# Kernel optimization log

Hardware: AMD Instinct MI355X
Metric: run time of the kernel (lower is better)

## Reference

```python
import jax, jax.numpy as jnp
import numpy as np

TOTAL_WORDS = 10000
EMBED_LEN = 100
SEQ_LEN = 80
BATCH = 2048
UNITS = 1024


def setup_inputs() -> dict:
    key = jax.random.key(0)
    ks = jax.random.split(key, 8)
    inputs = jax.random.randint(ks[0], (BATCH, SEQ_LEN), 0, TOTAL_WORDS)
    s = 0.02
    emb = jax.random.normal(ks[1], (TOTAL_WORDS, EMBED_LEN), jnp.float32) * s
    W0 = jax.random.normal(ks[2], (EMBED_LEN, 4 * UNITS), jnp.float32) * s
    U0 = jax.random.normal(ks[3], (UNITS, 4 * UNITS), jnp.float32) * s
    b0 = jnp.zeros((4 * UNITS,), jnp.float32)
    W1 = jax.random.normal(ks[4], (UNITS, 4 * UNITS), jnp.float32) * s
    U1 = jax.random.normal(ks[5], (UNITS, 4 * UNITS), jnp.float32) * s
    b1 = jnp.zeros((4 * UNITS,), jnp.float32)
    fcW = jax.random.normal(ks[6], (UNITS, 1), jnp.float32) * s
    fcb = jnp.zeros((1,), jnp.float32)
    return {"inputs": inputs, "emb": emb, "W0": W0, "U0": U0, "b0": b0,
            "W1": W1, "U1": U1, "b1": b1, "fcW": fcW, "fcb": fcb}


def _lstm_step(x, h, c, W, U, b):
    # Keras LSTMCell gate order: i, f, g(candidate), o
    z = x @ W + h @ U + b  # [B, 4*units]
    i, f, g, o = jnp.split(z, 4, axis=-1)
    i = jax.nn.sigmoid(i)
    f = jax.nn.sigmoid(f)
    g = jnp.tanh(g)
    o = jax.nn.sigmoid(o)
    c_new = f * c + i * g
    h_new = o * jnp.tanh(c_new)
    return h_new, c_new


def reference(inputs, emb, W0, U0, b0, W1, U1, b1, fcW, fcb):
    x = emb[inputs]                      # [B, T, E]
    xs = jnp.transpose(x, (1, 0, 2))     # [T, B, E] for scan over time
    B = inputs.shape[0]
    U = U0.shape[0]
    init = (jnp.zeros((B, U), x.dtype), jnp.zeros((B, U), x.dtype),
            jnp.zeros((B, U), x.dtype), jnp.zeros((B, U), x.dtype))

    def step(carry, xt):
        h0, c0, h1, c1 = carry
        h0, c0 = _lstm_step(xt, h0, c0, W0, U0, b0)
        h1, c1 = _lstm_step(h0, h1, c1, W1, U1, b1)
        return (h0, c0, h1, c1), None

    (h0, c0, h1, c1), _ = jax.lax.scan(step, init, xs)
    logits = h1 @ fcW + fcb              # [B, 1]
    return jax.nn.sigmoid(logits)
```

## Files before the change

kernel.cpp:

```cpp
#include <hip/hip_runtime.h>

#define DEVI __device__ __forceinline__

typedef __attribute__((ext_vector_type(4))) float f4;
typedef long long i64t;

DEVI unsigned char f2fp8(float x) {
  int p = __builtin_amdgcn_cvt_pk_fp8_f32(x, x, 0, false);
  return (unsigned char)(p & 0xff);
}
DEVI float fp82f(unsigned char b) {
  return __builtin_amdgcn_cvt_f32_fp8((int)b, 0);
}
DEVI float sigmoidf_(float x) { return 1.f / (1.f + __expf(-x)); }
DEVI float tanhf_(float x) {
  float ax = fabsf(x);
  float e = __expf(-2.f * ax);
  float t = (1.f - e) / (1.f + e);
  return x < 0.f ? -t : t;
}

#define GLDS16(g, l) __builtin_amdgcn_global_load_lds( \
    (const __attribute__((address_space(1))) void*)(g), \
    (__attribute__((address_space(3))) void*)(l), 16, 0, 0)

#define SCALE_UP 64.0f
#define SCALE_DN (1.0f / 4096.0f)


__global__ void k_conv_emb(const float* __restrict__ emb, unsigned char* __restrict__ ep) {
  int i = blockIdx.x * 256 + threadIdx.x;
  if (i >= 10000 * 128) return;
  int r = i >> 7, c = i & 127;
  ep[i] = (c < 100) ? f2fp8(emb[r * 100 + c] * SCALE_UP) : (unsigned char)0;
}

DEVI int permn(int n) {
  int g = n >> 10, u = n & 1023;
  return (u >> 5) * 128 + ((u >> 4) & 1) * 64 + g * 16 + (u & 15);
}
DEVI int kswz(int klog, int row) {
  return (klog & ~63) | ((((klog >> 4) & 3) ^ ((row >> 2) & 3)) << 4) | (klog & 15);
}

__global__ void k_conv_w0(const float* __restrict__ W0, const float* __restrict__ U0,
                          unsigned char* __restrict__ WT) {
  int i = blockIdx.x * 256 + threadIdx.x;
  if (i >= 4096 * 1152) return;
  int n = i / 1152, k = i - n * 1152;
  float v;
  if (k < 100) v = W0[k * 4096 + n];
  else if (k < 128) v = 0.f;
  else v = U0[(k - 128) * 4096 + n];
  int np = permn(n);
  WT[(size_t)np * 1152 + kswz(k, np)] = f2fp8(v * SCALE_UP);
}

__global__ void k_conv_w1(const float* __restrict__ W1, const float* __restrict__ U1,
                          unsigned char* __restrict__ WT) {
  int i = blockIdx.x * 256 + threadIdx.x;
  if (i >= 4096 * 2048) return;
  int n = i >> 11, k = i & 2047;
  float v = (k < 1024) ? W1[k * 4096 + n] : U1[(k - 1024) * 4096 + n];
  int np = permn(n);
  WT[(size_t)np * 2048 + kswz(k, np)] = f2fp8(v * SCALE_UP);
}


template<int K1, int KTOT, bool GATHER>
DEVI void lstm_body(int tile, char* smem,
    const unsigned char* __restrict__ src1,
    const unsigned char* __restrict__ src2,
    const int* __restrict__ idx, int t,
    const unsigned char* __restrict__ WT,
    const float* __restrict__ bias,
    float* __restrict__ cbuf,
    unsigned char* __restrict__ hout)
{
  const int tid = threadIdx.x;
  const int bn = tile & 31;
  const int bm = tile >> 5;
  const int m0 = bm * 256;
  const int n0 = bn * 128;

  const int lr = tid >> 2;
  const int c16 = (tid & 3) * 16;
  const int csw = (((tid & 3) ^ ((tid >> 4) & 3))) * 16;

  const unsigned char* g1[2];
  if (GATHER) {
#pragma unroll
    for (int p = 0; p < 2; ++p) {
      int w = idx[(m0 + p * 128 + lr) * 80 + t];
      g1[p] = src1 + (size_t)w * K1 + csw;
    }
  }

  char* const LA0 = smem;
  char* const LB0 = smem + 16384;
  char* const LA1 = smem + 24576;
  char* const LB1 = smem + 40960;

  auto stage = [&](int kb) {
    char* la = (kb & 1) ? LA1 : LA0;
    char* lb = (kb & 1) ? LB1 : LB0;
    const int kc = kb * 64;
    if (GATHER && kc < K1) {
#pragma unroll
      for (int p = 0; p < 2; ++p)
        GLDS16(g1[p] + kc, la + p * 8192 + tid * 16);
    } else {
#pragma unroll
      for (int p = 0; p < 2; ++p) {
        size_t row = (size_t)(m0 + p * 128 + lr);
        const unsigned char* g = (kc < K1)
            ? (src1 + row * 1024 + kc + c16)
            : (src2 + row * 1024 + (kc - K1) + c16);
        GLDS16(g, la + p * 8192 + tid * 16);
      }
    }
    GLDS16(WT + (size_t)(n0 + lr) * KTOT + kc + c16, lb + tid * 16);
  };

  const int lane = tid & 63;
  const int wv = tid >> 6;
  const int wm = wv >> 1;
  const int wn = wv & 1;
  const int cl = lane & 15;
  const int qd = lane >> 4;
  const int qh = qd >> 1, qb = qd & 1;
  const int fcl = (cl >> 2) & 3;
  const int koff0 = ((qh ^ fcl) << 4) + qb * 8;
  const int koff1 = (((2 + qh) ^ fcl) << 4) + qb * 8;

  f4 acc[4][4];
  const f4 fz = {0.f, 0.f, 0.f, 0.f};
#pragma unroll
  for (int a = 0; a < 4; ++a)
#pragma unroll
    for (int b = 0; b < 4; ++b) acc[a][b] = fz;

  stage(0);

  constexpr int NKB = KTOT / 64;
#pragma unroll 1
  for (int kb = 0; kb < NKB; ++kb) {
    __syncthreads();
    if (kb + 1 < NKB) stage(kb + 1);
    char* la = (kb & 1) ? LA1 : LA0;
    char* lb = (kb & 1) ? LB1 : LB0;
#pragma unroll
    for (int kk = 0; kk < 2; ++kk) {
      const int ko = kk ? koff1 : koff0;
      i64t af[4], bfr[4];
#pragma unroll
      for (int mi = 0; mi < 4; ++mi)
        af[mi] = *(const i64t*)(la + (wm * 64 + mi * 16 + cl) * 64 + ko);
#pragma unroll
      for (int j = 0; j < 4; ++j)
        bfr[j] = *(const i64t*)(lb + (wn * 64 + j * 16 + cl) * 64 + ko);
#pragma unroll
      for (int mi = 0; mi < 4; ++mi)
#pragma unroll
        for (int j = 0; j < 4; ++j)
          acc[mi][j] = __builtin_amdgcn_mfma_f32_16x16x32_fp8_fp8(
              af[mi], bfr[j], acc[mi][j], 0, 0, 0);
    }
  }

  const int u = bn * 32 + wn * 16 + cl;
  const int hcol = (u & ~63) | (((((u >> 4) & 3) ^ qd)) << 4) | (u & 15);
  const float bi = bias[u];
  const float bff = bias[1024 + u];
  const float bg = bias[2048 + u];
  const float bo = bias[3072 + u];
#pragma unroll
  for (int mi = 0; mi < 4; ++mi) {
    int mbase = m0 + wm * 64 + mi * 16 + qd * 4;
#pragma unroll
    for (int r = 0; r < 4; ++r) {
      int m = mbase + r;
      float gi = sigmoidf_(acc[mi][0][r] * SCALE_DN + bi);
      float gf = sigmoidf_(acc[mi][1][r] * SCALE_DN + bff);
      float gg = tanhf_(acc[mi][2][r] * SCALE_DN + bg);
      float go = sigmoidf_(acc[mi][3][r] * SCALE_DN + bo);
      size_t coff = (size_t)m * 1024 + u;
      float cn = gf * cbuf[coff] + gi * gg;
      cbuf[coff] = cn;
      hout[(size_t)m * 1024 + hcol] = f2fp8(go * tanhf_(cn) * SCALE_UP);
    }
  }
}

__global__ __launch_bounds__(512, 4) void k_step(
    int mode,
    const unsigned char* embp, const unsigned char* h0in,
    const int* idx, int t,
    const unsigned char* WT0, const float* b0, float* c0, unsigned char* h0out,
    const unsigned char* h0prev, const unsigned char* h1in,
    const unsigned char* WT1, const float* b1, float* c1, unsigned char* h1out)
{
  extern __shared__ char smem[];
  const int blk = blockIdx.x;
  int tile;
  bool isL0;
  if (mode == 1) {
    int hi = (blk >> 8) & 1;
    isL0 = ((blk & 1) ^ hi) != 0;
    tile = hi * 128 + ((blk & 255) >> 1);
  } else {
    tile = blk;
    isL0 = (mode == 0);
  }
  if (isL0)
    lstm_body<128, 1152, true>(tile, smem, embp, h0in, idx, t,
                               WT0, b0, c0, h0out);
  else
    lstm_body<1024, 2048, false>(tile, smem, h0prev, h1in, nullptr, 0,
                                 WT1, b1, c1, h1out);
}


__global__ void k_fc(const unsigned char* __restrict__ h1,
                     const float* __restrict__ fcW, const float* __restrict__ fcb,
                     float* __restrict__ out) {
  int wv = threadIdx.x >> 6;
  int lane = threadIdx.x & 63;
  int row = blockIdx.x * 4 + wv;
  if (row >= 2048) return;
  const unsigned char* hr = h1 + (size_t)row * 1024;
  const int f = (row >> 2) & 3;
  float s = 0.f;
  for (int k = lane; k < 1024; k += 64) {
    int ks = (k & ~63) | ((((k >> 4) & 3) ^ f) << 4) | (k & 15);
    s += fp82f(hr[ks]) * fcW[k];
  }
#pragma unroll
  for (int off = 32; off > 0; off >>= 1) s += __shfl_down(s, off);
  if (lane == 0) out[row] = sigmoidf_(s * (1.0f / SCALE_UP) + fcb[0]);
}


extern "C" void kernel_launch(void* const* d_in, const int* in_sizes, int n_in,
                              void* d_out, int out_size, void* d_ws, size_t ws_size,
                              hipStream_t stream) {
  const int*   idx = (const int*)d_in[0];
  const float* emb = (const float*)d_in[1];
  const float* W0  = (const float*)d_in[2];
  const float* U0  = (const float*)d_in[3];
  const float* b0  = (const float*)d_in[4];
  const float* W1  = (const float*)d_in[5];
  const float* U1  = (const float*)d_in[6];
  const float* b1  = (const float*)d_in[7];
  const float* fcW = (const float*)d_in[8];
  const float* fcb = (const float*)d_in[9];
  float* out = (float*)d_out;

  char* ws = (char*)d_ws;
  unsigned char* embp = (unsigned char*)(ws);
  unsigned char* WT0  = (unsigned char*)(ws + 1280000);
  unsigned char* WT1  = (unsigned char*)(ws + 5998592);
  unsigned char* h0b[2] = {(unsigned char*)(ws + 14387200),
                           (unsigned char*)(ws + 16484352)};
  unsigned char* h1b[2] = {(unsigned char*)(ws + 18581504),
                           (unsigned char*)(ws + 20678656)};
  float* c0 = (float*)(ws + 22775808);
  float* c1 = (float*)(ws + 31164416);

  hipMemsetAsync(ws + 14387200, 0, 25165824, stream);

  k_conv_emb<<<5000, 256, 0, stream>>>(emb, embp);
  k_conv_w0<<<18432, 256, 0, stream>>>(W0, U0, WT0);
  k_conv_w1<<<32768, 256, 0, stream>>>(W1, U1, WT1);

  k_step<<<256, 512, 49152, stream>>>(0, embp, h0b[1], idx, 0,
                                      WT0, b0, c0, h0b[0],
                                      nullptr, nullptr, WT1, b1, c1, nullptr);
  for (int t = 1; t < 80; ++t) {
    k_step<<<512, 512, 49152, stream>>>(1, embp, h0b[(t + 1) & 1], idx, t,
                                        WT0, b0, c0, h0b[t & 1],
                                        h0b[(t - 1) & 1], h1b[t & 1],
                                        WT1, b1, c1, h1b[(t + 1) & 1]);
  }
  k_step<<<256, 512, 49152, stream>>>(2, nullptr, nullptr, nullptr, 0,
                                      WT0, b0, c0, nullptr,
                                      h0b[1], h1b[0], WT1, b1, c1, h1b[1]);

  k_fc<<<512, 256, 0, stream>>>(h1b[1], fcW, fcb, out);
}
```

Before: 4.036 ms.

## Triple-buffer LDS staging with vmcnt waits and finer 8-byte XOR swizzle

Moves the GEMM K-loop from double to triple buffering in LDS, prefetching two stages ahead and using explicit s_waitcnt vmcnt plus s_barrier in place of __syncthreads. It also changes the weight and hidden-state swizzle from 16-byte to 8-byte XOR granularity to cut LDS bank conflicts on the 8-byte fragment reads, and raises MFMA priority with s_setprio. The cost is 72KB of LDS per block, which may lower occupancy. The hand-counted vmcnt values are fragile if the number of issued loads per stage changes.

```diff
diff --git a/kernel.cpp b/kernel.cpp
--- a/kernel.cpp
+++ b/kernel.cpp
@@ -40,7 +40,7 @@
   return (u >> 5) * 128 + ((u >> 4) & 1) * 64 + g * 16 + (u & 15);
 }
 DEVI int kswz(int klog, int row) {
-  return (klog & ~63) | ((((klog >> 4) & 3) ^ ((row >> 2) & 3)) << 4) | (klog & 15);
+  return (klog & ~63) | (((((klog >> 3) & 7) ^ ((row >> 1) & 7))) << 3) | (klog & 7);
 }
 
 __global__ void k_conv_w0(const float* __restrict__ W0, const float* __restrict__ U0,
@@ -85,7 +85,7 @@
 
   const int lr = tid >> 2;
   const int c16 = (tid & 3) * 16;
-  const int csw = (((tid & 3) ^ ((tid >> 4) & 3))) * 16;
+  const int csw = (((tid & 3) ^ ((tid >> 3) & 3))) * 16;
 
   const unsigned char* g1[2];
   if (GATHER) {
@@ -96,14 +96,13 @@
     }
   }
 
-  char* const LA0 = smem;
-  char* const LB0 = smem + 16384;
-  char* const LA1 = smem + 24576;
-  char* const LB1 = smem + 40960;
-
-  auto stage = [&](int kb) {
-    char* la = (kb & 1) ? LA1 : LA0;
-    char* lb = (kb & 1) ? LB1 : LB0;
+  char* const R0 = smem;
+  char* const R1 = smem + 24576;
+  char* const R2 = smem + 49152;
+
+  auto stage = [&](int kb, char* buf) {
+    char* la = buf;
+    char* lb = buf + 16384;
     const int kc = kb * 64;
     if (GATHER && kc < K1) {
 #pragma unroll
@@ -129,9 +128,12 @@
   const int cl = lane & 15;
   const int qd = lane >> 4;
   const int qh = qd >> 1, qb = qd & 1;
-  const int fcl = (cl >> 2) & 3;
-  const int koff0 = ((qh ^ fcl) << 4) + qb * 8;
-  const int koff1 = (((2 + qh) ^ fcl) << 4) + qb * 8;
+  const int g8s = (cl >> 1) & 7;
+  const int ko8_0 = ((0 + qd) ^ g8s) << 3;
+  const int ko8_1 = ((4 + qd) ^ g8s) << 3;
+  const int g4s = (cl >> 1) & 3;
+  const int ko16_0 = ((qh ^ g4s) << 4) + qb * 8;
+  const int ko16_1 = (((2 + qh) ^ g4s) << 4) + qb * 8;
 
   f4 acc[4][4];
   const f4 fz = {0.f, 0.f, 0.f, 0.f};
@@ -140,36 +142,55 @@
 #pragma unroll
     for (int b = 0; b < 4; ++b) acc[a][b] = fz;
 
-  stage(0);
+  stage(0, R0);
+  stage(1, R1);
 
   constexpr int NKB = KTOT / 64;
+  int rd = 0;
 #pragma unroll 1
   for (int kb = 0; kb < NKB; ++kb) {
-    __syncthreads();
-    if (kb + 1 < NKB) stage(kb + 1);
-    char* la = (kb & 1) ? LA1 : LA0;
-    char* lb = (kb & 1) ? LB1 : LB0;
+    if (kb == NKB - 1)
+      asm volatile("s_waitcnt vmcnt(0) lgkmcnt(0)" ::: "memory");
+    else
+      asm volatile("s_waitcnt vmcnt(3) lgkmcnt(0)" ::: "memory");
+    asm volatile("s_barrier" ::: "memory");
+
+    char* bufs[3] = {R0, R1, R2};
+    char* la = bufs[rd];
+    char* lb = la + 16384;
+    int st = rd + 2; if (st >= 3) st -= 3;
+    if (kb + 2 < NKB) stage(kb + 2, bufs[st]);
+
+    const bool A16 = GATHER && (kb * 64) < K1;
+    const int koA0 = A16 ? ko16_0 : ko8_0;
+    const int koA1 = A16 ? ko16_1 : ko8_1;
 #pragma unroll
     for (int kk = 0; kk < 2; ++kk) {
-      const int ko = kk ? koff1 : koff0;
+      const int koA = kk ? koA1 : koA0;
+      const int koB = kk ? ko8_1 : ko8_0;
       i64t af[4], bfr[4];
 #pragma unroll
       for (int mi = 0; mi < 4; ++mi)
-        af[mi] = *(const i64t*)(la + (wm * 64 + mi * 16 + cl) * 64 + ko);
+        af[mi] = *(const i64t*)(la + (wm * 64 + mi * 16 + cl) * 64 + koA);
 #pragma unroll
       for (int j = 0; j < 4; ++j)
-        bfr[j] = *(const i64t*)(lb + (wn * 64 + j * 16 + cl) * 64 + ko);
+        bfr[j] = *(const i64t*)(lb + (wn * 64 + j * 16 + cl) * 64 + koB);
+      __builtin_amdgcn_s_setprio(1);
 #pragma unroll
       for (int mi = 0; mi < 4; ++mi)
 #pragma unroll
         for (int j = 0; j < 4; ++j)
           acc[mi][j] = __builtin_amdgcn_mfma_f32_16x16x32_fp8_fp8(
               af[mi], bfr[j], acc[mi][j], 0, 0, 0);
+      __builtin_amdgcn_s_setprio(0);
     }
+    rd = rd + 1; if (rd >= 3) rd -= 3;
   }
 
   const int u = bn * 32 + wn * 16 + cl;
-  const int hcol = (u & ~63) | (((((u >> 4) & 3) ^ qd)) << 4) | (u & 15);
+  const int uhi = u & ~63;
+  const int uc8 = (u >> 3) & 7;
+  const int ulo = u & 7;
   const float bi = bias[u];
   const float bff = bias[1024 + u];
   const float bg = bias[2048 + u];
@@ -180,6 +201,8 @@
 #pragma unroll
     for (int r = 0; r < 4; ++r) {
       int m = mbase + r;
+      int fm = (qd * 2 + (r >> 1)) & 7;
+      int hcol = uhi | ((uc8 ^ fm) << 3) | ulo;
       float gi = sigmoidf_(acc[mi][0][r] * SCALE_DN + bi);
       float gf = sigmoidf_(acc[mi][1][r] * SCALE_DN + bff);
       float gg = tanhf_(acc[mi][2][r] * SCALE_DN + bg);
@@ -229,10 +252,10 @@
   int row = blockIdx.x * 4 + wv;
   if (row >= 2048) return;
   const unsigned char* hr = h1 + (size_t)row * 1024;
-  const int f = (row >> 2) & 3;
+  const int f = (row >> 1) & 7;
   float s = 0.f;
   for (int k = lane; k < 1024; k += 64) {
-    int ks = (k & ~63) | ((((k >> 4) & 3) ^ f) << 4) | (k & 15);
+    int ks = (k & ~63) | ((((k >> 3) & 7) ^ f) << 3) | (k & 7);
     s += fp82f(hr[ks]) * fcW[k];
   }
 #pragma unroll
@@ -273,16 +296,16 @@
   k_conv_w0<<<18432, 256, 0, stream>>>(W0, U0, WT0);
   k_conv_w1<<<32768, 256, 0, stream>>>(W1, U1, WT1);
 
-  k_step<<<256, 512, 49152, stream>>>(0, embp, h0b[1], idx, 0,
+  k_step<<<256, 512, 73728, stream>>>(0, embp, h0b[1], idx, 0,
                                       WT0, b0, c0, h0b[0],
                                       nullptr, nullptr, WT1, b1, c1, nullptr);
   for (int t = 1; t < 80; ++t) {
-    k_step<<<512, 512, 49152, stream>>>(1, embp, h0b[(t + 1) & 1], idx, t,
+    k_step<<<512, 512, 73728, stream>>>(1, embp, h0b[(t + 1) & 1], idx, t,
                                         WT0, b0, c0, h0b[t & 1],
                                         h0b[(t - 1) & 1], h1b[t & 1],
                                         WT1, b1, c1, h1b[(t + 1) & 1]);
   }
-  k_step<<<256, 512, 49152, stream>>>(2, nullptr, nullptr, nullptr, 0,
+  k_step<<<256, 512, 73728, stream>>>(2, nullptr, nullptr, nullptr, 0,
                                       WT0, b0, c0, nullptr,
                                       h0b[1], h1b[0], WT1, b1, c1, h1b[1]);
 
```

After: 6.005 ms. 48.8% more time.
